# Optimization experiments

Measured on AMD Instinct MI355X. Metric: run time of the kernel, lower is better.

## Reference

```python
import jax, jax.numpy as jnp
import numpy as np

B, N, D, H = 2, 2048, 128, 16  # batch, seq, per-head dim, heads
ALL = D * H


def setup_inputs() -> dict:
    key = jax.random.key(0)
    ks = jax.random.split(key, 12)
    s = 0.02
    x = jax.random.normal(ks[0], (B, N, D), dtype=jnp.float32)
    mask = jax.random.randint(ks[1], (B, N), 0, 2, dtype=jnp.int32)
    Wq = jax.random.normal(ks[2], (D, ALL), dtype=jnp.float32) * s
    bq = jnp.zeros((ALL,), dtype=jnp.float32)
    Wk = jax.random.normal(ks[3], (D, ALL), dtype=jnp.float32) * s
    bk = jnp.zeros((ALL,), dtype=jnp.float32)
    Wv = jax.random.normal(ks[4], (D, ALL), dtype=jnp.float32) * s
    bv = jnp.zeros((ALL,), dtype=jnp.float32)
    Wo = jax.random.normal(ks[5], (ALL, D), dtype=jnp.float32) * s
    bo = jnp.zeros((D,), dtype=jnp.float32)
    return {"x": x, "mask": mask, "Wq": Wq, "bq": bq, "Wk": Wk, "bk": bk,
            "Wv": Wv, "bv": bv, "Wo": Wo, "bo": bo}


def reference(x, mask, Wq, bq, Wk, bk, Wv, bv, Wo, bo):
    b, n, d = x.shape
    h = ALL // d
    # project and split heads: [b, n, h, d] -> [b, h, n, d]
    q = (x @ Wq + bq).reshape(b, n, h, d).transpose(0, 2, 1, 3)
    k = (x @ Wk + bk).reshape(b, n, h, d).transpose(0, 2, 1, 3)
    v = (x @ Wv + bv).reshape(b, n, h, d).transpose(0, 2, 1, 3)
    scores = jnp.einsum('bhqd,bhkd->bhqk', q, k) / jnp.sqrt(jnp.float32(d))
    # key mask: [b,1,1,n]
    scores = jnp.where(mask[:, None, None, :] == 0, -jnp.inf, scores)
    attn = jax.nn.softmax(scores, axis=-1)  # dropout p=0.0 -> identity
    out = jnp.einsum('bhqk,bhkd->bhqd', attn, v)
    # query mask: [b,1,n,1]
    out = jnp.where(mask[:, None, :, None] == 0, 0.0, out)
    out = out.transpose(0, 2, 1, 3).reshape(b, n, h * d)
    return out @ Wo + bo
```

## Files before the change

### kernel.cpp

```cpp
#include <hip/hip_runtime.h>
#include <hip/hip_bf16.h>

#define B_   2
#define N_   2048
#define D_   128
#define H_   16
#define ALL_ 2048
#define M_   (B_*N_)
#define BH_  (B_*H_)

typedef __bf16 bf16;
typedef __bf16 bf16x8 __attribute__((ext_vector_type(8)));
typedef __bf16 bf16x4 __attribute__((ext_vector_type(4)));
typedef float  floatx4 __attribute__((ext_vector_type(4)));

#define MFMA32K(a,b,c) __builtin_amdgcn_mfma_f32_16x16x32_bf16((a),(b),(c),0,0,0)

__device__ inline void load_lds16(const bf16* g, bf16* l) {
    __builtin_amdgcn_global_load_lds((const __attribute__((address_space(1))) void*)g,
                                     (__attribute__((address_space(3))) void*)l, 16, 0, 0);
}

#define WAITCNT_VM(n) ((0xF << 8) | (0x7 << 4) | (n))


__global__ __launch_bounds__(256) void prep_weights(const float* __restrict__ x,
                                                    const float* __restrict__ Wq,
                                                    const float* __restrict__ Wk,
                                                    const float* __restrict__ Wv,
                                                    const float* __restrict__ Wo,
                                                    const int* __restrict__ mask,
                                                    bf16* __restrict__ Wqf,
                                                    bf16* __restrict__ Wkf,
                                                    bf16* __restrict__ Wvf,
                                                    bf16* __restrict__ Wof,
                                                    bf16* __restrict__ xf,
                                                    float* __restrict__ mbias) {
    __shared__ bf16 pw[16896];
    int bid = blockIdx.x, t = threadIdx.x;
    int lane = t & 63, wave = t >> 6;
    int lrow = lane & 15, quad = lane >> 4;

    if (bid < 192) {
        int m = bid / 64, rest = bid % 64;
        int cg = rest >> 1, kh = rest & 1;
        const float* W = (m == 0) ? Wq : (m == 1) ? Wk : Wv;
        bf16* Wf       = (m == 0) ? Wqf : (m == 1) ? Wkf : Wvf;
        int slot = t & 15, rowb = t >> 4;
#pragma unroll
        for (int i = 0; i < 4; i++) {
            int rl_ = rowb + i * 16;
            float4 v = *(const float4*)(W + (size_t)(kh * 64 + rl_) * 2048 + cg * 64 + slot * 4);
            bf16x4 o; o[0]=(bf16)v.x; o[1]=(bf16)v.y; o[2]=(bf16)v.z; o[3]=(bf16)v.w;
            *(bf16x4*)(&pw[rl_ * 68 + slot * 4]) = o;
        }
        __syncthreads();
        int ctl = wave;
#pragma unroll
        for (int kfl = 0; kfl < 2; kfl++) {
            bf16x8 w;
#pragma unroll
            for (int j = 0; j < 8; j++) w[j] = pw[(kfl * 32 + quad * 8 + j) * 68 + ctl * 16 + lrow];
            *(bf16x8*)(Wf + (size_t)((cg * 4 + ctl) * 4 + kh * 2 + kfl) * 512 + lane * 8) = w;
        }
    } else if (bid < 224) {
        int idx = bid - 192;
        int kb16 = idx >> 1, ch = idx & 1;
        int k0 = kb16 * 128;
        int slot = t & 15, rowb = t >> 4;
#pragma unroll
        for (int i = 0; i < 8; i++) {
            int r = rowb + i * 16;
            float4 v = *(const float4*)(Wo + (size_t)(k0 + r) * 128 + ch * 64 + slot * 4);
            bf16x4 o; o[0]=(bf16)v.x; o[1]=(bf16)v.y; o[2]=(bf16)v.z; o[3]=(bf16)v.w;
            *(bf16x4*)(&pw[r * 68 + slot * 4]) = o;
        }
        __syncthreads();
        int ctl = wave;
        int ct = ch * 4 + ctl;
#pragma unroll
        for (int kfl = 0; kfl < 4; kfl++) {
            bf16x8 w;
#pragma unroll
            for (int j = 0; j < 8; j++)
                w[j] = pw[(kfl * 32 + ((j >> 2) << 4) + quad * 4 + (j & 3)) * 68 + ctl * 16 + lrow];
            *(bf16x8*)(Wof + (size_t)(ct * 64 + kb16 * 4 + kfl) * 512 + lane * 8) = w;
        }
    } else if (bid < 352) {
        int idx = bid - 224, r0 = idx * 32;
        int slot = t & 31, rowb = t >> 5;
#pragma unroll
        for (int i = 0; i < 4; i++) {
            int r = rowb + i * 8;
            float4 v = *(const float4*)(x + (size_t)(r0 + r) * 128 + slot * 4);
            bf16x4 o; o[0]=(bf16)v.x; o[1]=(bf16)v.y; o[2]=(bf16)v.z; o[3]=(bf16)v.w;
            *(bf16x4*)(&pw[r * 136 + slot * 4]) = o;
        }
        __syncthreads();
        int rtl = wave >> 1;
        int kf2 = (wave & 1) * 2;
#pragma unroll
        for (int kfl = 0; kfl < 2; kfl++) {
            int kf = kf2 + kfl;
            bf16x8 w = *(const bf16x8*)(&pw[(rtl * 16 + lrow) * 136 + kf * 32 + quad * 8]);
            *(bf16x8*)(xf + (size_t)((idx * 2 + rtl) * 4 + kf) * 512 + lane * 8) = w;
        }
    } else {
        int e = (bid - 352) * 256 + t;
        mbias[e] = mask[e] ? 0.0f : -43.2808512f;
    }
}

__global__ __launch_bounds__(256) void qkv_proj(const bf16* __restrict__ xf,
                                                const float* __restrict__ bq,
                                                const float* __restrict__ bk,
                                                const float* __restrict__ bv,
                                                const bf16* __restrict__ Wqf,
                                                const bf16* __restrict__ Wkf,
                                                const bf16* __restrict__ Wvf,
                                                bf16* __restrict__ Qf,
                                                bf16* __restrict__ Kf,
                                                bf16* __restrict__ Vf) {
    __shared__ bf16 tile[64][72];

    int tid = threadIdx.x;
    int wave = tid >> 6, lane = tid & 63;
    int lrow = lane & 15, quad = lane >> 4;
    int r0b = blockIdx.x * 64;
    int c0 = blockIdx.y * 64;
    int cg4 = c0 >> 4;

    int rt = (r0b >> 4) + wave;
    bf16x8 a[4];
#pragma unroll
    for (int kf = 0; kf < 4; kf++)
        a[kf] = *(const bf16x8*)(xf + (size_t)(rt * 4 + kf) * 512 + lane * 8);

    int bb = r0b >> 11;
    int h  = c0 >> 7;
    int bhw = bb * 16 + h;
    int tile16 = (r0b & 2047) >> 4;
    int kbt = (r0b & 2047) >> 6;
    floatx4 zero4 = {0.f, 0.f, 0.f, 0.f};

#pragma unroll
    for (int z = 0; z < 3; z++) {
        const float* bias = (z == 0) ? bq : (z == 1) ? bk : bv;
        const bf16*  Wf   = (z == 0) ? Wqf : (z == 1) ? Wkf : Wvf;

        floatx4 acc[4] = {zero4, zero4, zero4, zero4};
#pragma unroll
        for (int kf = 0; kf < 4; kf++) {
#pragma unroll
            for (int nf = 0; nf < 4; nf++) {
                bf16x8 b = *(const bf16x8*)(Wf + (size_t)((cg4 + nf) * 4 + kf) * 512 + lane * 8);
                acc[nf] = MFMA32K(a[kf], b, acc[nf]);
            }
        }

#pragma unroll
        for (int nf = 0; nf < 4; nf++) {
            int col = nf * 16 + lrow;
            float bvv = bias[c0 + col];
#pragma unroll
            for (int r = 0; r < 4; r++) {
                int row = wave * 16 + quad * 4 + r;
                bf16 val = (bf16)(acc[nf][r] + bvv);
                if (z < 2) tile[row][col] = val;
                else       tile[col][row] = val;
            }
        }
        __syncthreads();

        if (z < 2) {
            bf16* dst = (z == 0) ? Qf : Kf;
            int s = wave;
            int kfbase = (c0 & 127) >> 5;
            size_t fbase = ((size_t)bhw * 128 + tile16 + s) * 4 + kfbase;
#pragma unroll
            for (int kfl = 0; kfl < 2; kfl++) {
                bf16x8 w = *(const bf16x8*)(&tile[s * 16 + lrow][kfl * 32 + quad * 8]);
                *(bf16x8*)(dst + (fbase + kfl) * 512 + lane * 8) = w;
            }
        } else {
            int nfl = wave;
            int nfbase = (c0 & 127) >> 4;
            size_t fbase = (((size_t)bhw * 32 + kbt) * 8 + (nfbase + nfl)) * 2;
#pragma unroll
            for (int g = 0; g < 2; g++) {
                bf16x4 a0 = *(const bf16x4*)(&tile[nfl * 16 + lrow][g * 32 + quad * 4]);
                bf16x4 a1 = *(const bf16x4*)(&tile[nfl * 16 + lrow][g * 32 + 16 + quad * 4]);
                bf16x8 w;
                w[0]=a0[0]; w[1]=a0[1]; w[2]=a0[2]; w[3]=a0[3];
                w[4]=a1[0]; w[5]=a1[1]; w[6]=a1[2]; w[7]=a1[3];
                *(bf16x8*)(Vf + (fbase + g) * 512 + lane * 8) = w;
            }
        }
        if (z < 2) __syncthreads();
    }
}

__global__ __launch_bounds__(256, 2) void flash_attn(const bf16* __restrict__ Qf,
                                                     const bf16* __restrict__ Kf,
                                                     const bf16* __restrict__ Vf,
                                                     const float* __restrict__ mbias,
                                                     const int* __restrict__ mask,
                                                     bf16* __restrict__ ctxf) {
    __shared__ bf16 sm[20480];
    float* mbL = (float*)&sm[16384];

    int tid = threadIdx.x;
    int wave = tid >> 6, lane = tid & 63;
    int lrow = lane & 15, quad = lane >> 4;
    int bid = blockIdx.x;
    int xcd = bid & 7, seq = bid >> 3;
    int bh  = xcd * 4 + (seq >> 4);
    int qblk = seq & 15;
    int b  = bh >> 4;
    int q0 = qblk * 128 + wave * 32;

    const float* mbp = mbias + b * N_;
    const bf16* kbase = Kf + (size_t)bh * 262144;
    const bf16* vbase = Vf + (size_t)bh * 262144;

    bf16x8 qf[2][4];
#pragma unroll
    for (int u = 0; u < 2; u++)
#pragma unroll
        for (int kf = 0; kf < 4; kf++)
            qf[u][kf] = *(const bf16x8*)(Qf + (size_t)(((size_t)bh * 128 + (q0 >> 4) + u) * 4 + kf) * 512 + lane * 8);

    bf16x8 ones;
#pragma unroll
    for (int j = 0; j < 8; j++) ones[j] = (bf16)1.0f;

    floatx4 zero4 = {0.f, 0.f, 0.f, 0.f};
    floatx4 O[2][8];
#pragma unroll
    for (int u = 0; u < 2; u++)
#pragma unroll
        for (int nf = 0; nf < 8; nf++) O[u][nf] = zero4;
    floatx4 Oext[2] = {zero4, zero4};

    const float scale = 0.12751742f;

#pragma unroll
    for (int i = 0; i < 4; i++) {
        int seg = wave * 4 + i;
        load_lds16(kbase + seg * 512 + lane * 8, &sm[seg * 512]);
    }
#pragma unroll
    for (int i = 0; i < 2; i++) {
        int seg = wave * 2 + i;
        load_lds16((const bf16*)(mbp + seg * 256) + lane * 8, (bf16*)(mbL + seg * 256));
    }

    for (int kb = 0; kb < 32; kb++) {
        int cur = (kb & 1) << 13;

        __builtin_amdgcn_s_waitcnt(WAITCNT_VM(0));
        __builtin_amdgcn_s_barrier();

        if (kb < 31) {
            int nxt = cur ^ 8192;
            const bf16* ksrc = kbase + (size_t)(kb + 1) * 8192;
#pragma unroll
            for (int i = 0; i < 4; i++) {
                int seg = wave * 4 + i;
                load_lds16(ksrc + seg * 512 + lane * 8, &sm[nxt + seg * 512]);
            }
        }

        const bf16* vsrc = vbase + (size_t)kb * 8192 + lane * 8;
        bf16x8 vreg[16];
#pragma unroll
        for (int f = 0; f < 16; f++)
            vreg[f] = *(const bf16x8*)(vsrc + f * 512);

        bf16x8 pf[2][2];
#pragma unroll
        for (int s = 0; s < 4; s++) {
            floatx4 S0 = zero4, S1 = zero4;
            __builtin_amdgcn_s_setprio(1);
#pragma unroll
            for (int kf = 0; kf < 4; kf++) {
                bf16x8 kfr = *(const bf16x8*)(&sm[cur + ((s * 4 + kf) * 64 + lane) * 8]);
                S0 = MFMA32K(kfr, qf[0][kf], S0);
                S1 = MFMA32K(kfr, qf[1][kf], S1);
            }
            __builtin_amdgcn_s_setprio(0);
            float4 mb4 = *(const float4*)(mbL + kb * 64 + s * 16 + quad * 4);
            const float* mbr = (const float*)&mb4;
            int g = s >> 1, o = (s & 1) * 4;
#pragma unroll
            for (int r = 0; r < 4; r++) {
                float p0 = __builtin_amdgcn_exp2f(fmaf(S0[r], scale, mbr[r]));
                float p1 = __builtin_amdgcn_exp2f(fmaf(S1[r], scale, mbr[r]));
                pf[0][g][o + r] = (bf16)p0;
                pf[1][g][o + r] = (bf16)p1;
            }
        }

#pragma unroll
        for (int g = 0; g < 2; g++) {
            Oext[0] = MFMA32K(ones, pf[0][g], Oext[0]);
            Oext[1] = MFMA32K(ones, pf[1][g], Oext[1]);
        }

        __builtin_amdgcn_s_setprio(1);
#pragma unroll
        for (int nf = 0; nf < 8; nf++) {
#pragma unroll
            for (int g = 0; g < 2; g++) {
                O[0][nf] = MFMA32K(vreg[nf * 2 + g], pf[0][g], O[0][nf]);
                O[1][nf] = MFMA32K(vreg[nf * 2 + g], pf[1][g], O[1][nf]);
            }
        }
        __builtin_amdgcn_s_setprio(0);
    }

    const int* mp = mask + b * N_;
    int h4 = (bh & 15) * 4;
    size_t qtb = (size_t)b * 128 + (q0 >> 4);
#pragma unroll
    for (int u = 0; u < 2; u++) {
        float lsum = Oext[u][0];
        int q = q0 + u * 16 + lrow;
        float rl = (mp[q] && lsum > 0.f) ? (1.0f / lsum) : 0.f;
#pragma unroll
        for (int g = 0; g < 4; g++) {
            bf16x8 w;
#pragma unroll
            for (int j = 0; j < 4; j++) {
                w[j]     = (bf16)(O[u][2 * g][j]     * rl);
                w[j + 4] = (bf16)(O[u][2 * g + 1][j] * rl);
            }
            *(bf16x8*)(ctxf + ((qtb + u) * 64 + h4 + g) * 512 + lane * 8) = w;
        }
    }
}

__global__ __launch_bounds__(128) void out_proj(const bf16* __restrict__ ctxf,
                                                const bf16* __restrict__ Wof,
                                                const float* __restrict__ bo,
                                                float* __restrict__ out) {
    __shared__ float red[512];
    int tid = threadIdx.x;
    int wave = tid >> 6, lane = tid & 63;
    int lrow = lane & 15, quad = lane >> 4;
    int qt = blockIdx.x;
    int ct = blockIdx.y * 2;
    int r0 = qt * 16, c0 = ct * 16;

    floatx4 zero4 = {0.f, 0.f, 0.f, 0.f};
    floatx4 acc[2] = {zero4, zero4};
    const bf16* ap = ctxf + ((size_t)qt * 64 + wave * 32) * 512 + lane * 8;
    const bf16* b0 = Wof + ((size_t)ct * 64 + wave * 32) * 512 + lane * 8;
    const bf16* b1 = b0 + (size_t)64 * 512;
#pragma unroll 4
    for (int kf = 0; kf < 32; kf++) {
        bf16x8 a  = *(const bf16x8*)(ap + (size_t)kf * 512);
        bf16x8 w0 = *(const bf16x8*)(b0 + (size_t)kf * 512);
        bf16x8 w1 = *(const bf16x8*)(b1 + (size_t)kf * 512);
        acc[0] = MFMA32K(a, w0, acc[0]);
        acc[1] = MFMA32K(a, w1, acc[1]);
    }
    if (wave == 1) {
#pragma unroll
        for (int nf = 0; nf < 2; nf++)
#pragma unroll
            for (int r = 0; r < 4; r++)
                red[nf * 256 + r * 64 + lane] = acc[nf][r];
    }
    __syncthreads();
    if (wave == 0) {
#pragma unroll
        for (int nf = 0; nf < 2; nf++) {
            int col = c0 + nf * 16 + lrow;
            float bv = bo[col];
#pragma unroll
            for (int r = 0; r < 4; r++) {
                int m = r0 + quad * 4 + r;
                out[(size_t)m * 128 + col] = acc[nf][r] + red[nf * 256 + r * 64 + lane] + bv;
            }
        }
    }
}

extern "C" void kernel_launch(void* const* d_in, const int* in_sizes, int n_in,
                              void* d_out, int out_size, void* d_ws, size_t ws_size,
                              hipStream_t stream) {
    const float* x    = (const float*)d_in[0];
    const int*   mask = (const int*)d_in[1];
    const float* Wq   = (const float*)d_in[2];
    const float* bq   = (const float*)d_in[3];
    const float* Wk   = (const float*)d_in[4];
    const float* bk   = (const float*)d_in[5];
    const float* Wv   = (const float*)d_in[6];
    const float* bv   = (const float*)d_in[7];
    const float* Wo   = (const float*)d_in[8];
    const float* bo   = (const float*)d_in[9];
    float* out = (float*)d_out;

    char* ws = (char*)d_ws;
    size_t off = 0;
    bf16* Wqf = (bf16*)(ws + off); off += (size_t)262144 * 2;
    bf16* Wkf = (bf16*)(ws + off); off += (size_t)262144 * 2;
    bf16* Wvf = (bf16*)(ws + off); off += (size_t)262144 * 2;
    bf16* Wof = (bf16*)(ws + off); off += (size_t)262144 * 2;
    bf16* xf  = (bf16*)(ws + off); off += (size_t)524288 * 2;
    size_t qkv_elems = (size_t)BH_ * N_ * 128;
    bf16* Qf  = (bf16*)(ws + off); off += qkv_elems * 2;
    bf16* Kf  = (bf16*)(ws + off); off += qkv_elems * 2;
    bf16* Vf  = (bf16*)(ws + off); off += qkv_elems * 2;
    bf16* ctxf = (bf16*)(ws + off); off += (size_t)M_ * ALL_ * 2;
    float* mbias = (float*)(ws + off); off += (size_t)B_ * N_ * 4;
    (void)ws_size; (void)in_sizes; (void)n_in; (void)out_size;

    prep_weights<<<368, 256, 0, stream>>>(x, Wq, Wk, Wv, Wo, mask,
                                          Wqf, Wkf, Wvf, Wof, xf, mbias);

    qkv_proj<<<dim3(64, 32), 256, 0, stream>>>(xf, bq, bk, bv, Wqf, Wkf, Wvf,
                                               Qf, Kf, Vf);

    flash_attn<<<512, 256, 0, stream>>>(Qf, Kf, Vf, mbias, mask, ctxf);

    out_proj<<<dim3(256, 4), 128, 0, stream>>>(ctxf, Wof, bo, out);
}
```

Measured before the change: 173.0 us.

## Software-pipeline flash attention QK/softmax with PV and remap out_proj blocks per XCD

The flash attention loop now keeps K tiles in a 4-stage LDS ring, prefetching three tiles ahead. It computes the QK scores and exp for tile t+1 interleaved with the PV MFMAs for tile t, so softmax work can overlap matrix work and there is one barrier per iteration with a partial vmcnt wait. LDS use grows to 64KB plus a separate mask buffer, which may lower occupancy below the two-blocks launch bound, and register pressure rises from the double-buffered P fragments. The out_proj grid is flattened and remapped so that blocks sharing a row tile land on the same XCD, to improve L2 reuse.

```diff
diff --git a/kernel.cpp b/kernel.cpp
--- a/kernel.cpp
+++ b/kernel.cpp
@@ -206,8 +206,8 @@
                                                      const float* __restrict__ mbias,
                                                      const int* __restrict__ mask,
                                                      bf16* __restrict__ ctxf) {
-    __shared__ bf16 sm[20480];
-    float* mbL = (float*)&sm[16384];
+    __shared__ bf16 sm[32768];
+    __shared__ float mbL[2048];
 
     int tid = threadIdx.x;
     int wave = tid >> 6, lane = tid & 63;
@@ -221,7 +221,7 @@
 
     const float* mbp = mbias + b * N_;
     const bf16* kbase = Kf + (size_t)bh * 262144;
-    const bf16* vbase = Vf + (size_t)bh * 262144;
+    const bf16* vbase = Vf + (size_t)bh * 262144 + lane * 8;
 
     bf16x8 qf[2][4];
 #pragma unroll
@@ -245,78 +245,159 @@
     const float scale = 0.12751742f;
 
 #pragma unroll
-    for (int i = 0; i < 4; i++) {
-        int seg = wave * 4 + i;
-        load_lds16(kbase + seg * 512 + lane * 8, &sm[seg * 512]);
+    for (int tt = 0; tt < 3; tt++) {
+#pragma unroll
+        for (int i = 0; i < 4; i++) {
+            int seg = wave * 4 + i;
+            load_lds16(kbase + (size_t)tt * 8192 + seg * 512 + lane * 8,
+                       &sm[tt * 8192 + seg * 512]);
+        }
     }
 #pragma unroll
     for (int i = 0; i < 2; i++) {
         int seg = wave * 2 + i;
         load_lds16((const bf16*)(mbp + seg * 256) + lane * 8, (bf16*)(mbL + seg * 256));
     }
-
-    for (int kb = 0; kb < 32; kb++) {
-        int cur = (kb & 1) << 13;
-
-        __builtin_amdgcn_s_waitcnt(WAITCNT_VM(0));
-        __builtin_amdgcn_s_barrier();
-
-        if (kb < 31) {
-            int nxt = cur ^ 8192;
-            const bf16* ksrc = kbase + (size_t)(kb + 1) * 8192;
+    __builtin_amdgcn_s_waitcnt(WAITCNT_VM(0));
+    __builtin_amdgcn_s_barrier();
+
+    bf16x8 pa[2], pb[2];
+#pragma unroll
+    for (int s = 0; s < 4; s++) {
+        floatx4 S0 = zero4, S1 = zero4;
+        __builtin_amdgcn_s_setprio(1);
+#pragma unroll
+        for (int kf = 0; kf < 4; kf++) {
+            bf16x8 kfr = *(const bf16x8*)(&sm[((s * 4 + kf) * 64 + lane) * 8]);
+            S0 = MFMA32K(kfr, qf[0][kf], S0);
+            S1 = MFMA32K(kfr, qf[1][kf], S1);
+        }
+        __builtin_amdgcn_s_setprio(0);
+        float4 mb4 = *(const float4*)(mbL + s * 16 + quad * 4);
+        const float* mbr = (const float*)&mb4;
+        int o = (s & 1) * 4;
+#pragma unroll
+        for (int r = 0; r < 4; r++) {
+            float p0 = __builtin_amdgcn_exp2f(fmaf(S0[r], scale, mbr[r]));
+            float p1 = __builtin_amdgcn_exp2f(fmaf(S1[r], scale, mbr[r]));
+            if (s < 2) { pa[0][o + r] = (bf16)p0; pa[1][o + r] = (bf16)p1; }
+            else       { pb[0][o + r] = (bf16)p0; pb[1][o + r] = (bf16)p1; }
+        }
+    }
+
+    for (int t = 0; t < 32; t++) {
+        const bf16* vsrc = vbase + (size_t)t * 8192;
+        bf16x8 vreg[16];
+#pragma unroll
+        for (int f = 0; f < 16; f++)
+            vreg[f] = *(const bf16x8*)(vsrc + f * 512);
+
+        if (t < 29) {
+            int dst = ((t + 3) & 3) << 13;
+            const bf16* ksrc = kbase + (size_t)(t + 3) * 8192;
 #pragma unroll
             for (int i = 0; i < 4; i++) {
                 int seg = wave * 4 + i;
-                load_lds16(ksrc + seg * 512 + lane * 8, &sm[nxt + seg * 512]);
-            }
-        }
-
-        const bf16* vsrc = vbase + (size_t)kb * 8192 + lane * 8;
-        bf16x8 vreg[16];
-#pragma unroll
-        for (int f = 0; f < 16; f++)
-            vreg[f] = *(const bf16x8*)(vsrc + f * 512);
-
-        bf16x8 pf[2][2];
-#pragma unroll
-        for (int s = 0; s < 4; s++) {
-            floatx4 S0 = zero4, S1 = zero4;
+                load_lds16(ksrc + seg * 512 + lane * 8, &sm[dst + seg * 512]);
+            }
+        }
+
+        int nb = ((t + 1) & 3) << 13;
+        int tn = t + 1;
+        bf16x8 pan[2], pbn[2];
+        floatx4 Sa0, Sa1, Sb0, Sb1;
+
+        if (t < 31) {
+            Sa0 = zero4; Sa1 = zero4; Sb0 = zero4; Sb1 = zero4;
             __builtin_amdgcn_s_setprio(1);
 #pragma unroll
             for (int kf = 0; kf < 4; kf++) {
-                bf16x8 kfr = *(const bf16x8*)(&sm[cur + ((s * 4 + kf) * 64 + lane) * 8]);
-                S0 = MFMA32K(kfr, qf[0][kf], S0);
-                S1 = MFMA32K(kfr, qf[1][kf], S1);
+                bf16x8 kfr = *(const bf16x8*)(&sm[nb + ((0 * 4 + kf) * 64 + lane) * 8]);
+                Sa0 = MFMA32K(kfr, qf[0][kf], Sa0);
+                Sa1 = MFMA32K(kfr, qf[1][kf], Sa1);
+            }
+#pragma unroll
+            for (int kf = 0; kf < 4; kf++) {
+                bf16x8 kfr = *(const bf16x8*)(&sm[nb + ((1 * 4 + kf) * 64 + lane) * 8]);
+                Sb0 = MFMA32K(kfr, qf[0][kf], Sb0);
+                Sb1 = MFMA32K(kfr, qf[1][kf], Sb1);
             }
             __builtin_amdgcn_s_setprio(0);
-            float4 mb4 = *(const float4*)(mbL + kb * 64 + s * 16 + quad * 4);
+            float4 mb4 = *(const float4*)(mbL + tn * 64 + 0 * 16 + quad * 4);
             const float* mbr = (const float*)&mb4;
-            int g = s >> 1, o = (s & 1) * 4;
 #pragma unroll
             for (int r = 0; r < 4; r++) {
-                float p0 = __builtin_amdgcn_exp2f(fmaf(S0[r], scale, mbr[r]));
-                float p1 = __builtin_amdgcn_exp2f(fmaf(S1[r], scale, mbr[r]));
-                pf[0][g][o + r] = (bf16)p0;
-                pf[1][g][o + r] = (bf16)p1;
-            }
-        }
-
-#pragma unroll
-        for (int g = 0; g < 2; g++) {
-            Oext[0] = MFMA32K(ones, pf[0][g], Oext[0]);
-            Oext[1] = MFMA32K(ones, pf[1][g], Oext[1]);
+                pan[0][r] = (bf16)__builtin_amdgcn_exp2f(fmaf(Sa0[r], scale, mbr[r]));
+                pan[1][r] = (bf16)__builtin_amdgcn_exp2f(fmaf(Sa1[r], scale, mbr[r]));
+            }
         }
 
         __builtin_amdgcn_s_setprio(1);
+        Oext[0] = MFMA32K(ones, pa[0], Oext[0]);
+        Oext[1] = MFMA32K(ones, pa[1], Oext[1]);
 #pragma unroll
         for (int nf = 0; nf < 8; nf++) {
-#pragma unroll
-            for (int g = 0; g < 2; g++) {
-                O[0][nf] = MFMA32K(vreg[nf * 2 + g], pf[0][g], O[0][nf]);
-                O[1][nf] = MFMA32K(vreg[nf * 2 + g], pf[1][g], O[1][nf]);
-            }
+            O[0][nf] = MFMA32K(vreg[nf * 2], pa[0], O[0][nf]);
+            O[1][nf] = MFMA32K(vreg[nf * 2], pa[1], O[1][nf]);
         }
         __builtin_amdgcn_s_setprio(0);
+
+        if (t < 31) {
+            float4 mb4 = *(const float4*)(mbL + tn * 64 + 1 * 16 + quad * 4);
+            const float* mbr = (const float*)&mb4;
+#pragma unroll
+            for (int r = 0; r < 4; r++) {
+                pan[0][4 + r] = (bf16)__builtin_amdgcn_exp2f(fmaf(Sb0[r], scale, mbr[r]));
+                pan[1][4 + r] = (bf16)__builtin_amdgcn_exp2f(fmaf(Sb1[r], scale, mbr[r]));
+            }
+            Sa0 = zero4; Sa1 = zero4; Sb0 = zero4; Sb1 = zero4;
+            __builtin_amdgcn_s_setprio(1);
+#pragma unroll
+            for (int kf = 0; kf < 4; kf++) {
+                bf16x8 kfr = *(const bf16x8*)(&sm[nb + ((2 * 4 + kf) * 64 + lane) * 8]);
+                Sa0 = MFMA32K(kfr, qf[0][kf], Sa0);
+                Sa1 = MFMA32K(kfr, qf[1][kf], Sa1);
+            }
+#pragma unroll
+            for (int kf = 0; kf < 4; kf++) {
+                bf16x8 kfr = *(const bf16x8*)(&sm[nb + ((3 * 4 + kf) * 64 + lane) * 8]);
+                Sb0 = MFMA32K(kfr, qf[0][kf], Sb0);
+                Sb1 = MFMA32K(kfr, qf[1][kf], Sb1);
+            }
+            __builtin_amdgcn_s_setprio(0);
+            float4 mb4b = *(const float4*)(mbL + tn * 64 + 2 * 16 + quad * 4);
+            const float* mbr2 = (const float*)&mb4b;
+#pragma unroll
+            for (int r = 0; r < 4; r++) {
+                pbn[0][r] = (bf16)__builtin_amdgcn_exp2f(fmaf(Sa0[r], scale, mbr2[r]));
+                pbn[1][r] = (bf16)__builtin_amdgcn_exp2f(fmaf(Sa1[r], scale, mbr2[r]));
+            }
+        }
+
+        __builtin_amdgcn_s_setprio(1);
+        Oext[0] = MFMA32K(ones, pb[0], Oext[0]);
+        Oext[1] = MFMA32K(ones, pb[1], Oext[1]);
+#pragma unroll
+        for (int nf = 0; nf < 8; nf++) {
+            O[0][nf] = MFMA32K(vreg[nf * 2 + 1], pb[0], O[0][nf]);
+            O[1][nf] = MFMA32K(vreg[nf * 2 + 1], pb[1], O[1][nf]);
+        }
+        __builtin_amdgcn_s_setprio(0);
+
+        if (t < 31) {
+            float4 mb4 = *(const float4*)(mbL + tn * 64 + 3 * 16 + quad * 4);
+            const float* mbr = (const float*)&mb4;
+#pragma unroll
+            for (int r = 0; r < 4; r++) {
+                pbn[0][4 + r] = (bf16)__builtin_amdgcn_exp2f(fmaf(Sb0[r], scale, mbr[r]));
+                pbn[1][4 + r] = (bf16)__builtin_amdgcn_exp2f(fmaf(Sb1[r], scale, mbr[r]));
+            }
+#pragma unroll
+            for (int u = 0; u < 2; u++) { pa[u] = pan[u]; pb[u] = pbn[u]; }
+        }
+
+        __builtin_amdgcn_s_waitcnt(WAITCNT_VM(4));
+        __builtin_amdgcn_s_barrier();
     }
 
     const int* mp = mask + b * N_;
@@ -348,8 +429,10 @@
     int tid = threadIdx.x;
     int wave = tid >> 6, lane = tid & 63;
     int lrow = lane & 15, quad = lane >> 4;
-    int qt = blockIdx.x;
-    int ct = blockIdx.y * 2;
+    int bid = blockIdx.x;
+    int xcd = bid & 7, idx = bid >> 3;
+    int qt = xcd * 32 + (idx >> 2);
+    int ct = (idx & 3) * 2;
     int r0 = qt * 16, c0 = ct * 16;
 
     floatx4 zero4 = {0.f, 0.f, 0.f, 0.f};
@@ -425,5 +508,5 @@
 
     flash_attn<<<512, 256, 0, stream>>>(Qf, Kf, Vf, mbias, mask, ctxf);
 
-    out_proj<<<dim3(256, 4), 128, 0, stream>>>(ctxf, Wof, bo, out);
+    out_proj<<<1024, 128, 0, stream>>>(ctxf, Wof, bo, out);
 }
```

Measured after the change: 176.4 us. About the same (+2.0%).
